# Kernel tuning notes

Measured on AMD Instinct MI355X. Metric: run time of the kernel, lower is better.

Reference implementation:

```python
import jax, jax.numpy as jnp
import numpy as np

D_MODEL = 1024
B, T_Q, T_KV = 4, 2048, 2048


def _linear_params(key, d_in, d_out):
    kw, kb = jax.random.split(key)
    W = jax.random.normal(kw, (d_out, d_in), dtype=jnp.float32) * 0.02
    b = jax.random.normal(kb, (d_out,), dtype=jnp.float32) * 0.02
    return W, b


def setup_inputs() -> dict:
    key = jax.random.key(0)
    ks = jax.random.split(key, 7)
    latent_space = jax.random.normal(ks[0], (B, T_Q, D_MODEL), dtype=jnp.float32)
    input_space = jax.random.normal(ks[1], (B, T_KV, D_MODEL), dtype=jnp.float32)
    Wl, bl = _linear_params(ks[2], D_MODEL, D_MODEL)
    Wu, bu = _linear_params(ks[3], D_MODEL, D_MODEL)
    WA, bA = _linear_params(ks[4], D_MODEL, D_MODEL)  # A_proj: d -> J (J = d)
    WV, bV = _linear_params(ks[5], D_MODEL, D_MODEL)  # V_proj: J -> d
    Wo, bo = _linear_params(ks[6], D_MODEL, D_MODEL)
    return {
        "latent_space": latent_space, "input_space": input_space,
        "Wl": Wl, "bl": bl, "Wu": Wu, "bu": bu,
        "WA": WA, "bA": bA, "WV": WV, "bV": bV,
        "Wo": Wo, "bo": bo,
    }


def reference(latent_space, input_space, Wl, bl, Wu, bu, WA, bA, WV, bV, Wo, bo):
    # emb_0 = l_proj(latent)            [B, T_q, d]
    emb0 = jnp.einsum('bqd,ed->bqe', latent_space, Wl) + bl
    # l = softmax(u_proj(emb_0), -1)^T  [B, d, T_q]
    l = jax.nn.softmax(jnp.einsum('bqd,ed->bqe', emb0, Wu) + bu, axis=-1)
    l = jnp.swapaxes(l, -2, -1)
    # D = A_proj(input)                 [B, T_kv, J]
    Dm = jnp.einsum('bkd,jd->bkj', input_space, WA) + bA
    # A = softmax(V_proj(D), dim=-2)    softmax over T_kv
    A = jax.nn.softmax(jnp.einsum('bkj,dj->bkd', Dm, WV) + bV, axis=-2)
    # w = A @ l                         [B, T_kv, T_q]
    w = jnp.einsum('bkd,bdq->bkq', A, l)
    # o = w @ o_proj(latent)            [B, T_kv, d]
    ov = jnp.einsum('bqd,ed->bqe', latent_space, Wo) + bo
    o = jnp.einsum('bkq,bqd->bkd', w, ov)
    return o
```

## Files before the change

### kernel.cpp

```cpp
#include <hip/hip_runtime.h>
#include <hip/hip_bf16.h>
#include <stdint.h>

typedef __attribute__((ext_vector_type(8))) short bf16x8;
typedef __attribute__((ext_vector_type(4))) float f32x4;
typedef __attribute__((ext_vector_type(4))) unsigned short u16x4;

#define B_  4
#define T_  2048
#define D_  1024
#define BM  128
#define BN  128
#define BK  32

__device__ __forceinline__ float bf2f(ushort u) {
  union { unsigned int i; float f; } v; v.i = ((unsigned int)u) << 16; return v.f;
}
__device__ __forceinline__ ushort f2bf(float f) {
  return (ushort)(__bfloat16_as_ushort(__float2bfloat16(f)));
}
__device__ __forceinline__ void async16(const void* g, void* l) {
  __builtin_amdgcn_global_load_lds(
      (const __attribute__((address_space(1))) void*)g,
      (__attribute__((address_space(3))) void*)l, 16, 0, 0);
}
__device__ __forceinline__ int swz4(int r) { return (r ^ (r >> 2)) & 3; }

__global__ __launch_bounds__(256)
void prep(const float* __restrict__ lat, const float* __restrict__ inp,
          const float* __restrict__ Wl, const float* __restrict__ bl,
          const float* __restrict__ Wu, const float* __restrict__ bu,
          const float* __restrict__ WA, const float* __restrict__ bA,
          const float* __restrict__ WV, const float* __restrict__ bV,
          const float* __restrict__ Wo, const float* __restrict__ bo,
          ushort* __restrict__ xBf, ushort* __restrict__ xBf2,
          ushort* __restrict__ w1, ushort* __restrict__ w2,
          ushort* __restrict__ wCatWo, float* __restrict__ bc, float* __restrict__ bc2)
{
  __shared__ alignas(16) ushort t[64 * 65];
  const long NW = (long)D_ * D_;
  const int bx = blockIdx.x;
  const int tid = threadIdx.x;
  if (bx < 16384) {
    const float* in = bx < 8192 ? lat : inp;
    ushort* out = bx < 8192 ? xBf : xBf2;
    const long i = (long)(bx & 8191) * 256 + tid;
    const float4 v = *(const float4*)(in + i * 4);
    u16x4 o;
    o[0] = f2bf(v.x); o[1] = f2bf(v.y); o[2] = f2bf(v.z); o[3] = f2bf(v.w);
    *(u16x4*)(out + i * 4) = o;
  } else if (bx < 19456) {
    const int seg = (bx - 16384) >> 10;
    const float* in  = seg == 0 ? Wu : (seg == 1 ? WV : Wo);
    ushort* out = seg == 0 ? w1 : (seg == 1 ? w1 + NW : wCatWo);
    const long i = (long)((bx - 16384) & 1023) * 256 + tid;
    const float4 v = *(const float4*)(in + i * 4);
    u16x4 o;
    o[0] = f2bf(v.x); o[1] = f2bf(v.y); o[2] = f2bf(v.z); o[3] = f2bf(v.w);
    *(u16x4*)(out + i * 4) = o;
  } else if (bx < 19968) {
    const int z = (bx - 19456) >> 8;
    const int w = (bx - 19456) & 255;
    const float* in = z ? WA : Wl;
    ushort* out = z ? w2 + NW : w2;
    const int c0 = (w & 15) * 64, r0 = (w >> 4) * 64;
    const int tx = tid & 15, ty = tid >> 4;
#pragma unroll
    for (int i = 0; i < 4; ++i) {
      const int r = ty + i * 16;
      const float4 v = *(const float4*)(in + (long)(r0 + r) * D_ + c0 + tx * 4);
      t[(tx * 4 + 0) * 65 + r] = f2bf(v.x);
      t[(tx * 4 + 1) * 65 + r] = f2bf(v.y);
      t[(tx * 4 + 2) * 65 + r] = f2bf(v.z);
      t[(tx * 4 + 3) * 65 + r] = f2bf(v.w);
    }
    __syncthreads();
#pragma unroll
    for (int i = 0; i < 4; ++i) {
      const int c = ty + i * 16;
      u16x4 v;
#pragma unroll
      for (int j = 0; j < 4; ++j) v[j] = t[c * 65 + tx * 4 + j];
      *(u16x4*)(out + (long)(c0 + c) * D_ + r0 + tx * 4) = v;
    }
  } else {
    const int z = (bx - 19968) >> 8;
    const int w = (bx - 19968) & 255;
    const float* W    = z ? WV : Wu;
    const float* bin  = z ? bA : bl;
    const float* badd = z ? bV : bu;
    float* out        = z ? bc2 : bc;
    const int wv = tid >> 6, lane = tid & 63;
    const int e = w * 4 + wv;
    const float* row = W + (long)e * D_;
    float s = 0.f;
#pragma unroll
    for (int i = 0; i < 16; ++i) s += row[lane + i * 64] * bin[lane + i * 64];
#pragma unroll
    for (int off = 32; off; off >>= 1) s += __shfl_xor(s, off);
    if (lane == 0) out[e] = s + badd[e];
  }
}

template<bool OUT_F32, bool HAS_BIAS, bool EXP_OUT>
__global__ __launch_bounds__(256, 2)
void gemm_nt(const ushort* __restrict__ A, const ushort* __restrict__ B,
             const float* __restrict__ bias, void* __restrict__ C,
             int N, int K, long sA, long sB, long sC)
{
  __shared__ alignas(16) ushort As[BM * BK];
  __shared__ alignas(16) ushort Bs[BN * BK];
  const int tid  = threadIdx.x;
  const int wave = tid >> 6;
  const int lane = tid & 63;
  const int wm   = wave >> 1;
  const int wn   = wave & 1;
  const int bz   = blockIdx.z;
  const int tileN = blockIdx.x * BN;
  const int tileM = blockIdx.y * BM;
  A += (long)bz * sA;
  B += (long)bz * sB;

  const int lrow   = lane >> 2;
  const int lchunk = (lane & 3) ^ swz4(lrow);

  f32x4 acc[4][4];
#pragma unroll
  for (int i = 0; i < 4; ++i)
#pragma unroll
    for (int j = 0; j < 4; ++j) acc[i][j] = (f32x4){0.f, 0.f, 0.f, 0.f};

  const int frow = lane & 15;
  const int kg   = lane >> 4;
  const int coff = ((kg ^ swz4(frow)) << 3);

  for (int kt = 0; kt < K; kt += BK) {
    __syncthreads();
#pragma unroll
    for (int i = 0; i < 2; ++i) {
      const int rg  = wave * 2 + i;
      const int row = rg * 16 + lrow;
      async16(A + (long)(tileM + row) * K + kt + lchunk * 8, (void*)(As + rg * 16 * BK));
      async16(B + (long)(tileN + row) * K + kt + lchunk * 8, (void*)(Bs + rg * 16 * BK));
    }
    __syncthreads();
    bf16x8 af[4], bfr[4];
#pragma unroll
    for (int mi = 0; mi < 4; ++mi)
      af[mi] = *(const bf16x8*)(As + (wm * 64 + mi * 16 + frow) * BK + coff);
#pragma unroll
    for (int ni = 0; ni < 4; ++ni)
      bfr[ni] = *(const bf16x8*)(Bs + (wn * 64 + ni * 16 + frow) * BK + coff);
#pragma unroll
    for (int mi = 0; mi < 4; ++mi)
#pragma unroll
      for (int ni = 0; ni < 4; ++ni)
        acc[mi][ni] = __builtin_amdgcn_mfma_f32_16x16x32_bf16(af[mi], bfr[ni], acc[mi][ni], 0, 0, 0);
  }

  const int rowbase = tileM + wm * 64 + ((lane >> 4) << 2);
  const int colbase = tileN + wn * 64 + (lane & 15);
#pragma unroll
  for (int ni = 0; ni < 4; ++ni) {
    const int col = colbase + ni * 16;
    float bv = 0.f;
    if constexpr (HAS_BIAS) bv = bias[col];
#pragma unroll
    for (int mi = 0; mi < 4; ++mi) {
#pragma unroll
      for (int r = 0; r < 4; ++r) {
        const int row = rowbase + mi * 16 + r;
        float v = acc[mi][ni][r] + bv;
        if constexpr (EXP_OUT) v = __expf(v);
        const long idx = (long)bz * sC + (long)row * N + col;
        if constexpr (OUT_F32) ((float*)C)[idx] = v;
        else ((ushort*)C)[idx] = f2bf(v);
      }
    }
  }
}

template<int NB, int MODE>
__global__ __launch_bounds__(512, 2)
void gemm8(const ushort* __restrict__ A, const ushort* __restrict__ Bm,
           const float* __restrict__ bias1, const float* __restrict__ bias2,
           void* __restrict__ C1, void* __restrict__ C2,
           int ldA, int ldB, long sAz, long sBz, long sCz)
{
  constexpr int LPT = 2 + NB / 128;
  constexpr int WN  = NB / 64;
  constexpr int WM  = 8 / WN;
  constexpr int MR  = 256 / (16 * WM);
  constexpr int MW  = 256 / WM;
  constexpr int MH  = MR / 2;

  __shared__ alignas(16) ushort Ab[4][256 * 32];
  __shared__ alignas(16) ushort Bb[4][NB * 32];

  const int gx = gridDim.x, gy = gridDim.y;
  const int nwg = gx * gy * gridDim.z;
  int fid = (blockIdx.z * gy + blockIdx.y) * gx + blockIdx.x;
  fid = (fid & 7) * (nwg >> 3) + (fid >> 3);
  const int bx = fid % gx;
  const int by = (fid / gx) % gy;
  const int bz = fid / (gx * gy);

  const int tileM = by * 256, tileN = bx * NB;

  const ushort* Ap = A;
  const ushort* Bp = Bm;
  if constexpr (MODE == 2) {
    Ap += (long)(bz >> 1) * sAz + (long)(bz & 1) * 1024;
    Bp += (long)(bz >> 1) * sBz + (long)(bz & 1) * 1024;
  } else {
    Ap += (long)bz * sAz;
    Bp += (long)bz * sBz;
  }

  const int tid  = threadIdx.x;
  const int wid  = tid >> 6;
  const int lane = tid & 63;
  const int wm   = wid / WN;
  const int wn   = wid % WN;

  const int srow = tid >> 2;
  const int scol = (((tid & 3) ^ ((tid >> 3) & 3)) << 3);
  const ushort* gA0 = Ap + (long)(tileM + srow) * ldA + scol;
  const ushort* gA1 = Ap + (long)(tileM + 128 + srow) * ldA + scol;
  const ushort* gB0 = Bp + (long)(tileN + srow) * ldB + scol;
  const ushort* gB1 = (NB == 256) ? (Bp + (long)(tileN + 128 + srow) * ldB + scol) : gB0;
  const int wofs = wid << 9;

  const int frow  = lane & 15;
  const int cofs  = (((lane >> 4) ^ ((lane >> 1) & 3)) << 3);
  const int abase = wm * MW + frow;
  const int bbase = wn * 64 + frow;

  f32x4 acc[MR][4];
#pragma unroll
  for (int i = 0; i < MR; ++i)
#pragma unroll
    for (int j = 0; j < 4; ++j) acc[i][j] = (f32x4){0.f, 0.f, 0.f, 0.f};

#pragma unroll
  for (int p = 0; p < 3; ++p) {
    const int kt = p * 32;
    async16(gA0 + kt, Ab[p] + wofs);
    async16(gA1 + kt, Ab[p] + 4096 + wofs);
    async16(gB0 + kt, Bb[p] + wofs);
    if constexpr (NB == 256) async16(gB1 + kt, Bb[p] + 4096 + wofs);
  }
  if constexpr (LPT == 4) asm volatile("s_waitcnt vmcnt(8)" ::: "memory");
  else                    asm volatile("s_waitcnt vmcnt(6)" ::: "memory");
  __builtin_amdgcn_s_barrier();

  for (int t = 0; t < 32; ++t) {
    const int cur = t & 3;
    const int nxt = (t + 3) & 3;
    const int kt3 = (t + 3) * 32;
    const bool st = (t < 29);
    const ushort* __restrict__ Ac = Ab[cur];
    const ushort* __restrict__ Bc = Bb[cur];

    bf16x8 bf[4], af[MH];
#pragma unroll
    for (int ni = 0; ni < 4; ++ni)
      bf[ni] = *(const bf16x8*)(Bc + (bbase + ni * 16) * 32 + cofs);
#pragma unroll
    for (int mi = 0; mi < MH; ++mi)
      af[mi] = *(const bf16x8*)(Ac + (abase + mi * 16) * 32 + cofs);
    if (st) {
      async16(gA0 + kt3, Ab[nxt] + wofs);
      async16(gB0 + kt3, Bb[nxt] + wofs);
    }
    __builtin_amdgcn_s_barrier();
    __builtin_amdgcn_s_setprio(1);
#pragma unroll
    for (int mi = 0; mi < MH; ++mi)
#pragma unroll
      for (int ni = 0; ni < 4; ++ni)
        acc[mi][ni] = __builtin_amdgcn_mfma_f32_16x16x32_bf16(af[mi], bf[ni], acc[mi][ni], 0, 0, 0);
    __builtin_amdgcn_s_setprio(0);
    __builtin_amdgcn_s_barrier();

    bf16x8 ag[MH];
#pragma unroll
    for (int mi = 0; mi < MH; ++mi)
      ag[mi] = *(const bf16x8*)(Ac + (abase + (MH + mi) * 16) * 32 + cofs);
    if (st) {
      async16(gA1 + kt3, Ab[nxt] + 4096 + wofs);
      if constexpr (NB == 256) async16(gB1 + kt3, Bb[nxt] + 4096 + wofs);
    }
    __builtin_amdgcn_s_barrier();
    __builtin_amdgcn_s_setprio(1);
#pragma unroll
    for (int mi = 0; mi < MH; ++mi)
#pragma unroll
      for (int ni = 0; ni < 4; ++ni)
        acc[MH + mi][ni] = __builtin_amdgcn_mfma_f32_16x16x32_bf16(ag[mi], bf[ni], acc[MH + mi][ni], 0, 0, 0);
    __builtin_amdgcn_s_setprio(0);
    if (t < 29) {
      if constexpr (LPT == 4) asm volatile("s_waitcnt vmcnt(8)" ::: "memory");
      else                    asm volatile("s_waitcnt vmcnt(6)" ::: "memory");
    } else if (t == 29) {
      if constexpr (LPT == 4) asm volatile("s_waitcnt vmcnt(4)" ::: "memory");
      else                    asm volatile("s_waitcnt vmcnt(3)" ::: "memory");
    } else if (t == 30) {
      asm volatile("s_waitcnt vmcnt(0)" ::: "memory");
    }
    __builtin_amdgcn_s_barrier();
  }

  const int rowbase  = tileM + wm * MW + ((lane >> 4) << 2);
  const int colbase0 = wn * 64 + (lane & 15);

  if constexpr (MODE == 0) {
    const bool second = tileN >= 1024;
    ushort* Cp = (ushort*)(second ? C2 : C1);
    const float* bb = second ? bias2 : bias1;
    const int cb = tileN - (second ? 1024 : 0) + colbase0;
#pragma unroll
    for (int ni = 0; ni < 4; ++ni) {
      const int col = cb + ni * 16;
      const float bv = bb[col];
#pragma unroll
      for (int mi = 0; mi < MR; ++mi)
#pragma unroll
        for (int r = 0; r < 4; ++r)
          Cp[(long)(rowbase + mi * 16 + r) * 1024 + col] = f2bf(acc[mi][ni][r] + bv);
    }
  } else if constexpr (MODE == 1) {
    ushort* Cp = (ushort*)C1;
    const int cb = tileN + colbase0;
#pragma unroll
    for (int ni = 0; ni < 4; ++ni) {
      const int col = cb + ni * 16;
      const float bv = bias1[col];
#pragma unroll
      for (int mi = 0; mi < MR; ++mi)
#pragma unroll
        for (int r = 0; r < 4; ++r)
          Cp[(long)(rowbase + mi * 16 + r) * 1024 + col] = f2bf(__expf(acc[mi][ni][r] + bv));
    }
  } else if constexpr (MODE == 2) {
    ushort* Cp = (ushort*)C1 + ((long)(bz & 1) * B_ + (bz >> 1)) * ((long)D_ * D_);
    const int cb = tileN + colbase0;
#pragma unroll
    for (int ni = 0; ni < 4; ++ni) {
      const int col = cb + ni * 16;
#pragma unroll
      for (int mi = 0; mi < MR; ++mi)
#pragma unroll
        for (int r = 0; r < 4; ++r)
          Cp[(long)(rowbase + mi * 16 + r) * 1024 + col] = f2bf(acc[mi][ni][r]);
    }
  } else {
    float* Cp = (float*)C1 + (long)bz * sCz;
    const int cb = tileN + colbase0;
#pragma unroll
    for (int ni = 0; ni < 4; ++ni) {
      const int col = cb + ni * 16;
#pragma unroll
      for (int mi = 0; mi < MR; ++mi)
#pragma unroll
        for (int r = 0; r < 4; ++r)
          Cp[(long)(rowbase + mi * 16 + r) * 1024 + col] = acc[mi][ni][r];
    }
  }
}

__global__ __launch_bounds__(256)
void reduce2_scale(const ushort* __restrict__ P, const float* __restrict__ cinv,
                   ushort* __restrict__ MT)
{
  const long stride = (long)B_ * D_ * D_;
  const long base = ((long)blockIdx.x * 256 + threadIdx.x) * 8;
  const int b = (int)(base >> 20);
  const int e0 = (int)(base & (D_ - 1));
  bf16x8 p0 = *(const bf16x8*)(P + base);
  bf16x8 p1 = *(const bf16x8*)(P + stride + base);
  const float4 c0 = *(const float4*)(cinv + (long)b * D_ + e0);
  const float4 c1 = *(const float4*)(cinv + (long)b * D_ + e0 + 4);
  const float cc[8] = {c0.x, c0.y, c0.z, c0.w, c1.x, c1.y, c1.z, c1.w};
  bf16x8 o;
#pragma unroll
  for (int j = 0; j < 8; ++j)
    o[j] = (short)f2bf((bf2f((ushort)p0[j]) + bf2f((ushort)p1[j])) * cc[j]);
  *(bf16x8*)(MT + base) = o;
}

__global__ __launch_bounds__(256)
void softmax_row(ushort* __restrict__ S)
{
  const long base = (long)blockIdx.x * D_;
  const int tid = threadIdx.x;
  float e[4], s = 0.f;
#pragma unroll
  for (int i = 0; i < 4; ++i) { e[i] = __expf(bf2f(S[base + i * 256 + tid])); s += e[i]; }
#pragma unroll
  for (int off = 32; off; off >>= 1) s += __shfl_xor(s, off);
  __shared__ float reds[4];
  if ((tid & 63) == 0) reds[tid >> 6] = s;
  __syncthreads();
  s = reds[0] + reds[1] + reds[2] + reds[3];
  const float inv = 1.f / s;
#pragma unroll
  for (int i = 0; i < 4; ++i)
    S[base + i * 256 + tid] = f2bf(e[i] * inv);
}

__global__ __launch_bounds__(256)
void transpose2(const ushort* __restrict__ l, ushort* __restrict__ lT,
                const ushort* __restrict__ ov, ushort* __restrict__ ovT)
{
  __shared__ alignas(16) ushort t[64 * 65];
  const int z = blockIdx.z;
  const int b = z & (B_ - 1);
  const ushort* in = (z < B_ ? l : ov) + (long)b * T_ * D_;
  ushort* out      = (z < B_ ? lT : ovT) + (long)b * (long)D_ * T_;
  const int c0 = blockIdx.x * 64, r0 = blockIdx.y * 64;
  const int tx = threadIdx.x & 15, ty = threadIdx.x >> 4;
#pragma unroll
  for (int i = 0; i < 4; ++i) {
    const int r = ty + i * 16;
    u16x4 v = *(const u16x4*)(in + (long)(r0 + r) * D_ + c0 + tx * 4);
#pragma unroll
    for (int c = 0; c < 4; ++c) t[(tx * 4 + c) * 65 + r] = v[c];
  }
  __syncthreads();
#pragma unroll
  for (int i = 0; i < 4; ++i) {
    const int c = ty + i * 16;
    u16x4 v;
#pragma unroll
    for (int j = 0; j < 4; ++j) v[j] = t[c * 65 + tx * 4 + j];
    *(u16x4*)(out + (long)(c0 + c) * T_ + r0 + tx * 4) = v;
  }
}

__global__ __launch_bounds__(256)
void colsum_part(const ushort* __restrict__ E, float* __restrict__ psum)
{
  const int d = blockIdx.x * 256 + threadIdx.x;
  const int c = blockIdx.y;
  const int b = blockIdx.z;
  const ushort* p = E + ((long)b * T_ + (long)c * 128) * D_ + d;
  float s = 0.f;
#pragma unroll 4
  for (int r = 0; r < 128; ++r) s += bf2f(p[(long)r * D_]);
  psum[((long)b * 16 + c) * D_ + d] = s;
}

__global__ __launch_bounds__(256)
void colsum_comb(const float* __restrict__ psum, float* __restrict__ cinv)
{
  const int d = blockIdx.x * 256 + threadIdx.x;
  const int b = blockIdx.y;
  float s = 0.f;
#pragma unroll
  for (int c = 0; c < 16; ++c) s += psum[((long)b * 16 + c) * D_ + d];
  cinv[(long)b * D_ + d] = 1.f / s;
}

extern "C" void kernel_launch(void* const* d_in, const int* in_sizes, int n_in,
                              void* d_out, int out_size, void* d_ws, size_t ws_size,
                              hipStream_t stream)
{
  (void)in_sizes; (void)n_in; (void)out_size; (void)ws_size;
  const float* lat = (const float*)d_in[0];
  const float* inp = (const float*)d_in[1];
  const float* Wl  = (const float*)d_in[2];
  const float* bl  = (const float*)d_in[3];
  const float* Wu  = (const float*)d_in[4];
  const float* bu  = (const float*)d_in[5];
  const float* WA  = (const float*)d_in[6];
  const float* bA  = (const float*)d_in[7];
  const float* WV  = (const float*)d_in[8];
  const float* bV  = (const float*)d_in[9];
  const float* Wo  = (const float*)d_in[10];
  const float* bo  = (const float*)d_in[11];

  char* w = (char*)d_ws;
  auto carve = [&](size_t bytes) { char* p = w; w += (bytes + 255) & ~(size_t)255; return p; };
  const long NT = (long)B_ * T_ * D_;
  const long NW = (long)D_ * D_;
  ushort* xBf   = (ushort*)carve(NT * 2);
  ushort* xBf2  = (ushort*)carve(NT * 2);
  ushort* bufA  = (ushort*)carve(NT * 2);
  ushort* bufB  = (ushort*)carve(NT * 2);
  ushort* scr   = (ushort*)carve(NT * 2);
  ushort* MT    = (ushort*)carve((long)B_ * NW * 2);
  ushort* wCat  = (ushort*)carve(3 * NW * 2);
  float*  bc    = (float*)carve(D_ * 4);
  float*  bc2   = (float*)carve(D_ * 4);
  float*  psum  = (float*)carve(64 * 1024 * 4);
  float*  cinv  = (float*)carve(8 * 1024 * 4);
  ushort* w1 = scr;
  ushort* w2 = scr + 2 * NW;
  ushort* ovT = scr;
  ushort* part = bufB;

  const dim3 blk(256, 1, 1);
  const dim3 blk5(512, 1, 1);

  prep<<<dim3(20480), blk, 0, stream>>>(lat, inp, Wl, bl, Wu, bu, WA, bA, WV, bV, Wo, bo,
                                        xBf, xBf2, w1, w2, wCat + NW, bc, bc2);
  gemm_nt<false, false, false><<<dim3(8, 8, 2), blk, 0, stream>>>(
      w1, w2, nullptr, wCat, D_, D_, NW, NW, 2 * NW);
  gemm8<256, 0><<<dim3(8, 32, 1), blk5, 0, stream>>>(
      xBf, wCat, bc, bo, bufB, bufA, D_, D_, 0, 0, 0);
  softmax_row<<<dim3(B_ * T_), blk, 0, stream>>>(bufB);
  transpose2<<<dim3(16, 32, 2 * B_), blk, 0, stream>>>(bufB, xBf, bufA, ovT);
  gemm8<128, 2><<<dim3(8, 4, 8), blk5, 0, stream>>>(
      ovT, xBf, nullptr, nullptr, part, nullptr, T_, T_, (long)D_ * T_, (long)D_ * T_, 0);
  gemm8<128, 1><<<dim3(8, 32, 1), blk5, 0, stream>>>(
      xBf2, wCat + 2 * NW, bc2, nullptr, bufA, nullptr, D_, D_, 0, 0, 0);
  colsum_part<<<dim3(4, 16, B_), blk, 0, stream>>>(bufA, psum);
  colsum_comb<<<dim3(4, B_, 1), blk, 0, stream>>>(psum, cinv);
  reduce2_scale<<<dim3(2048), blk, 0, stream>>>(part, cinv, MT);
  gemm8<128, 3><<<dim3(8, 8, 4), blk5, 0, stream>>>(
      bufA, MT, nullptr, nullptr, d_out, nullptr, D_, D_,
      (long)T_ * D_, NW, (long)T_ * D_);
}
```

Before: 330.8 us.

## Restructure gemm8 main loop with register double-buffered fragments and single barrier per k-step

Rewrites the gemm8 K loop so that LDS fragments for the next k-tile are loaded into a second register set while MFMAs run on the current one, with one barrier per step instead of three. All global prefetches for a stage are issued together after the wait. The NB=256 variant is removed, so the first projection GEMM now uses 128-wide N tiles with twice as many workgroups. The aim is to cut barrier stalls and overlap LDS reads with MFMA work, at the cost of more registers for the duplicated fragment sets.

After: 359.2 us. 8.6% more time.

```diff
diff --git a/kernel.cpp b/kernel.cpp
--- a/kernel.cpp
+++ b/kernel.cpp
@@ -180,22 +180,15 @@
   }
 }
 
-template<int NB, int MODE>
+template<int MODE>
 __global__ __launch_bounds__(512, 2)
 void gemm8(const ushort* __restrict__ A, const ushort* __restrict__ Bm,
            const float* __restrict__ bias1, const float* __restrict__ bias2,
            void* __restrict__ C1, void* __restrict__ C2,
            int ldA, int ldB, long sAz, long sBz, long sCz)
 {
-  constexpr int LPT = 2 + NB / 128;
-  constexpr int WN  = NB / 64;
-  constexpr int WM  = 8 / WN;
-  constexpr int MR  = 256 / (16 * WM);
-  constexpr int MW  = 256 / WM;
-  constexpr int MH  = MR / 2;
-
   __shared__ alignas(16) ushort Ab[4][256 * 32];
-  __shared__ alignas(16) ushort Bb[4][NB * 32];
+  __shared__ alignas(16) ushort Bb[4][128 * 32];
 
   const int gx = gridDim.x, gy = gridDim.y;
   const int nwg = gx * gy * gridDim.z;
@@ -205,7 +198,7 @@
   const int by = (fid / gx) % gy;
   const int bz = fid / (gx * gy);
 
-  const int tileM = by * 256, tileN = bx * NB;
+  const int tileM = by * 256, tileN = bx * 128;
 
   const ushort* Ap = A;
   const ushort* Bp = Bm;
@@ -220,25 +213,24 @@
   const int tid  = threadIdx.x;
   const int wid  = tid >> 6;
   const int lane = tid & 63;
-  const int wm   = wid / WN;
-  const int wn   = wid % WN;
+  const int wm   = wid >> 1;
+  const int wn   = wid & 1;
 
   const int srow = tid >> 2;
   const int scol = (((tid & 3) ^ ((tid >> 3) & 3)) << 3);
   const ushort* gA0 = Ap + (long)(tileM + srow) * ldA + scol;
   const ushort* gA1 = Ap + (long)(tileM + 128 + srow) * ldA + scol;
   const ushort* gB0 = Bp + (long)(tileN + srow) * ldB + scol;
-  const ushort* gB1 = (NB == 256) ? (Bp + (long)(tileN + 128 + srow) * ldB + scol) : gB0;
   const int wofs = wid << 9;
 
   const int frow  = lane & 15;
   const int cofs  = (((lane >> 4) ^ ((lane >> 1) & 3)) << 3);
-  const int abase = wm * MW + frow;
+  const int abase = wm * 64 + frow;
   const int bbase = wn * 64 + frow;
 
-  f32x4 acc[MR][4];
-#pragma unroll
-  for (int i = 0; i < MR; ++i)
+  f32x4 acc[4][4];
+#pragma unroll
+  for (int i = 0; i < 4; ++i)
 #pragma unroll
     for (int j = 0; j < 4; ++j) acc[i][j] = (f32x4){0.f, 0.f, 0.f, 0.f};
 
@@ -248,70 +240,57 @@
     async16(gA0 + kt, Ab[p] + wofs);
     async16(gA1 + kt, Ab[p] + 4096 + wofs);
     async16(gB0 + kt, Bb[p] + wofs);
-    if constexpr (NB == 256) async16(gB1 + kt, Bb[p] + 4096 + wofs);
-  }
-  if constexpr (LPT == 4) asm volatile("s_waitcnt vmcnt(8)" ::: "memory");
-  else                    asm volatile("s_waitcnt vmcnt(6)" ::: "memory");
+  }
+  asm volatile("s_waitcnt vmcnt(6)" ::: "memory");
   __builtin_amdgcn_s_barrier();
 
-  for (int t = 0; t < 32; ++t) {
-    const int cur = t & 3;
-    const int nxt = (t + 3) & 3;
-    const int kt3 = (t + 3) * 32;
-    const bool st = (t < 29);
-    const ushort* __restrict__ Ac = Ab[cur];
-    const ushort* __restrict__ Bc = Bb[cur];
-
-    bf16x8 bf[4], af[MH];
-#pragma unroll
-    for (int ni = 0; ni < 4; ++ni)
-      bf[ni] = *(const bf16x8*)(Bc + (bbase + ni * 16) * 32 + cofs);
-#pragma unroll
-    for (int mi = 0; mi < MH; ++mi)
-      af[mi] = *(const bf16x8*)(Ac + (abase + mi * 16) * 32 + cofs);
-    if (st) {
-      async16(gA0 + kt3, Ab[nxt] + wofs);
-      async16(gB0 + kt3, Bb[nxt] + wofs);
-    }
-    __builtin_amdgcn_s_barrier();
-    __builtin_amdgcn_s_setprio(1);
-#pragma unroll
-    for (int mi = 0; mi < MH; ++mi)
-#pragma unroll
-      for (int ni = 0; ni < 4; ++ni)
-        acc[mi][ni] = __builtin_amdgcn_mfma_f32_16x16x32_bf16(af[mi], bf[ni], acc[mi][ni], 0, 0, 0);
-    __builtin_amdgcn_s_setprio(0);
-    __builtin_amdgcn_s_barrier();
-
-    bf16x8 ag[MH];
-#pragma unroll
-    for (int mi = 0; mi < MH; ++mi)
-      ag[mi] = *(const bf16x8*)(Ac + (abase + (MH + mi) * 16) * 32 + cofs);
-    if (st) {
-      async16(gA1 + kt3, Ab[nxt] + 4096 + wofs);
-      if constexpr (NB == 256) async16(gB1 + kt3, Bb[nxt] + 4096 + wofs);
-    }
-    __builtin_amdgcn_s_barrier();
-    __builtin_amdgcn_s_setprio(1);
-#pragma unroll
-    for (int mi = 0; mi < MH; ++mi)
-#pragma unroll
-      for (int ni = 0; ni < 4; ++ni)
-        acc[MH + mi][ni] = __builtin_amdgcn_mfma_f32_16x16x32_bf16(ag[mi], bf[ni], acc[MH + mi][ni], 0, 0, 0);
-    __builtin_amdgcn_s_setprio(0);
-    if (t < 29) {
-      if constexpr (LPT == 4) asm volatile("s_waitcnt vmcnt(8)" ::: "memory");
-      else                    asm volatile("s_waitcnt vmcnt(6)" ::: "memory");
-    } else if (t == 29) {
-      if constexpr (LPT == 4) asm volatile("s_waitcnt vmcnt(4)" ::: "memory");
-      else                    asm volatile("s_waitcnt vmcnt(3)" ::: "memory");
-    } else if (t == 30) {
-      asm volatile("s_waitcnt vmcnt(0)" ::: "memory");
-    }
-    __builtin_amdgcn_s_barrier();
-  }
-
-  const int rowbase  = tileM + wm * MW + ((lane >> 4) << 2);
+  bf16x8 f0a[4], f0b[4], f1a[4], f1b[4];
+#pragma unroll
+  for (int ni = 0; ni < 4; ++ni)
+    f0b[ni] = *(const bf16x8*)(Bb[0] + (bbase + ni * 16) * 32 + cofs);
+#pragma unroll
+  for (int mi = 0; mi < 4; ++mi)
+    f0a[mi] = *(const bf16x8*)(Ab[0] + (abase + mi * 16) * 32 + cofs);
+
+#define KSTEP(FC, FN, TC)                                                     \
+  {                                                                           \
+    if ((TC) == 30) { asm volatile("s_waitcnt vmcnt(0)" ::: "memory"); }      \
+    else            { asm volatile("s_waitcnt vmcnt(3)" ::: "memory"); }      \
+    __builtin_amdgcn_s_barrier();                                             \
+    if ((TC) + 3 < 32) {                                                      \
+      const int kt = ((TC) + 3) * 32; const int sl = ((TC) + 3) & 3;          \
+      async16(gA0 + kt, Ab[sl] + wofs);                                       \
+      async16(gA1 + kt, Ab[sl] + 4096 + wofs);                                \
+      async16(gB0 + kt, Bb[sl] + wofs);                                       \
+    }                                                                         \
+    if ((TC) + 1 < 32) {                                                      \
+      const int sl = ((TC) + 1) & 3;                                          \
+      _Pragma("unroll")                                                       \
+      for (int ni = 0; ni < 4; ++ni)                                          \
+        FN##b[ni] = *(const bf16x8*)(Bb[sl] + (bbase + ni * 16) * 32 + cofs); \
+      _Pragma("unroll")                                                       \
+      for (int mi = 0; mi < 4; ++mi)                                          \
+        FN##a[mi] = *(const bf16x8*)(Ab[sl] + (abase + mi * 16) * 32 + cofs); \
+    }                                                                         \
+    __builtin_amdgcn_sched_barrier(0);                                        \
+    __builtin_amdgcn_s_setprio(1);                                            \
+    _Pragma("unroll")                                                         \
+    for (int mi = 0; mi < 4; ++mi)                                            \
+      _Pragma("unroll")                                                       \
+      for (int ni = 0; ni < 4; ++ni)                                          \
+        acc[mi][ni] = __builtin_amdgcn_mfma_f32_16x16x32_bf16(                \
+            FC##a[mi], FC##b[ni], acc[mi][ni], 0, 0, 0);                      \
+    __builtin_amdgcn_s_setprio(0);                                            \
+  }
+
+#pragma unroll 1
+  for (int t = 0; t < 32; t += 2) {
+    KSTEP(f0, f1, t);
+    KSTEP(f1, f0, t + 1);
+  }
+#undef KSTEP
+
+  const int rowbase  = tileM + wm * 64 + ((lane >> 4) << 2);
   const int colbase0 = wn * 64 + (lane & 15);
 
   if constexpr (MODE == 0) {
@@ -324,7 +303,7 @@
       const int col = cb + ni * 16;
       const float bv = bb[col];
 #pragma unroll
-      for (int mi = 0; mi < MR; ++mi)
+      for (int mi = 0; mi < 4; ++mi)
 #pragma unroll
         for (int r = 0; r < 4; ++r)
           Cp[(long)(rowbase + mi * 16 + r) * 1024 + col] = f2bf(acc[mi][ni][r] + bv);
@@ -337,7 +316,7 @@
       const int col = cb + ni * 16;
       const float bv = bias1[col];
 #pragma unroll
-      for (int mi = 0; mi < MR; ++mi)
+      for (int mi = 0; mi < 4; ++mi)
 #pragma unroll
         for (int r = 0; r < 4; ++r)
           Cp[(long)(rowbase + mi * 16 + r) * 1024 + col] = f2bf(__expf(acc[mi][ni][r] + bv));
@@ -349,7 +328,7 @@
     for (int ni = 0; ni < 4; ++ni) {
       const int col = cb + ni * 16;
 #pragma unroll
-      for (int mi = 0; mi < MR; ++mi)
+      for (int mi = 0; mi < 4; ++mi)
 #pragma unroll
         for (int r = 0; r < 4; ++r)
           Cp[(long)(rowbase + mi * 16 + r) * 1024 + col] = f2bf(acc[mi][ni][r]);
@@ -361,7 +340,7 @@
     for (int ni = 0; ni < 4; ++ni) {
       const int col = cb + ni * 16;
 #pragma unroll
-      for (int mi = 0; mi < MR; ++mi)
+      for (int mi = 0; mi < 4; ++mi)
 #pragma unroll
         for (int r = 0; r < 4; ++r)
           Cp[(long)(rowbase + mi * 16 + r) * 1024 + col] = acc[mi][ni][r];
@@ -507,18 +486,18 @@
                                         xBf, xBf2, w1, w2, wCat + NW, bc, bc2);
   gemm_nt<false, false, false><<<dim3(8, 8, 2), blk, 0, stream>>>(
       w1, w2, nullptr, wCat, D_, D_, NW, NW, 2 * NW);
-  gemm8<256, 0><<<dim3(8, 32, 1), blk5, 0, stream>>>(
+  gemm8<0><<<dim3(16, 32, 1), blk5, 0, stream>>>(
       xBf, wCat, bc, bo, bufB, bufA, D_, D_, 0, 0, 0);
   softmax_row<<<dim3(B_ * T_), blk, 0, stream>>>(bufB);
   transpose2<<<dim3(16, 32, 2 * B_), blk, 0, stream>>>(bufB, xBf, bufA, ovT);
-  gemm8<128, 2><<<dim3(8, 4, 8), blk5, 0, stream>>>(
+  gemm8<2><<<dim3(8, 4, 8), blk5, 0, stream>>>(
       ovT, xBf, nullptr, nullptr, part, nullptr, T_, T_, (long)D_ * T_, (long)D_ * T_, 0);
-  gemm8<128, 1><<<dim3(8, 32, 1), blk5, 0, stream>>>(
+  gemm8<1><<<dim3(8, 32, 1), blk5, 0, stream>>>(
       xBf2, wCat + 2 * NW, bc2, nullptr, bufA, nullptr, D_, D_, 0, 0, 0);
   colsum_part<<<dim3(4, 16, B_), blk, 0, stream>>>(bufA, psum);
   colsum_comb<<<dim3(4, B_, 1), blk, 0, stream>>>(psum, cinv);
   reduce2_scale<<<dim3(2048), blk, 0, stream>>>(part, cinv, MT);
-  gemm8<128, 3><<<dim3(8, 8, 4), blk5, 0, stream>>>(
+  gemm8<3><<<dim3(8, 8, 4), blk5, 0, stream>>>(
       bufA, MT, nullptr, nullptr, d_out, nullptr, D_, D_,
       (long)T_ * D_, NW, (long)T_ * D_);
 }
```
